# Kernel tuning notes

Hardware: AMD Instinct MI355X
Metric: run time of the kernel (lower is better)

The kernel has to match this reference:

```python
import jax, jax.numpy as jnp
import numpy as np

B, T, C = 8, 2048, 512

def setup_inputs() -> dict:
    key = jax.random.key(0)
    ks = jax.random.split(key, 16)
    def n(k, shape, s=0.02):
        return jax.random.normal(k, shape, dtype=jnp.float32) * s
    inp = {
        'x_l': jax.random.normal(ks[0], (B, T, C), jnp.float32),
        'x_r': jax.random.normal(ks[1], (B, T, C), jnp.float32),
    }
    i = 2
    for name in ['lp1', 'rp1', 'lp2', 'rp2']:
        inp[name + '_w1'] = n(ks[i], (C, C))       # pointwise conv1d weight (out,in)
        inp[name + '_b1'] = jnp.zeros((C,), jnp.float32)
        inp[name + '_w2'] = n(ks[i + 1], (C, 3))   # depthwise conv k=3 weight per channel
        inp[name + '_b2'] = jnp.zeros((C,), jnp.float32)
        i += 2
    inp['lp3_w'] = n(ks[i], (C, C)); inp['lp3_b'] = jnp.zeros((C,), jnp.float32)
    inp['rp3_w'] = n(ks[i + 1], (C, C)); inp['rp3_b'] = jnp.zeros((C,), jnp.float32)
    return inp

def _proj(x, w1, b1, w2, b2):
    # x: (B,T,C). Pointwise conv1d (1x1) then depthwise conv1d k=3, pad=1 over T.
    h = jnp.einsum('btc,dc->btd', x, w1) + b1
    hp = jnp.pad(h, ((0, 0), (1, 1), (0, 0)))
    # cross-correlation: tap 0 -> t-1, tap 1 -> t, tap 2 -> t+1 (matches torch Conv1d)
    return hp[:, :-2, :] * w2[:, 0] + hp[:, 1:-1, :] * w2[:, 1] + hp[:, 2:, :] * w2[:, 2] + b2

def reference(x_l, x_r,
              lp1_w1, lp1_b1, lp1_w2, lp1_b2,
              rp1_w1, rp1_b1, rp1_w2, rp1_b2,
              lp2_w1, lp2_b1, lp2_w2, lp2_b2,
              rp2_w1, rp2_b1, rp2_w2, rp2_b2,
              lp3_w, lp3_b, rp3_w, rp3_b):
    scale = C ** (-0.5)
    Q_l = _proj(x_l, lp1_w1, lp1_b1, lp1_w2, lp1_b2)  # (B,T,C)
    Q_r = _proj(x_r, rp1_w1, rp1_b1, rp1_w2, rp1_b2)  # (B,T,C)
    V_l = _proj(x_l, lp2_w1, lp2_b1, lp2_w2, lp2_b2)  # (B,T,C)
    V_r = _proj(x_r, rp2_w1, rp2_b1, rp2_w2, rp2_b2)  # (B,T,C)
    attn = jnp.einsum('btc,bsc->bts', Q_l, Q_r) * scale  # shared (B,T,T) scores
    # r->l: softmax over r-positions (last axis)
    F_r2l = jnp.einsum('bts,bsc->btc', jax.nn.softmax(attn, axis=-1), V_r)
    # l->r: softmax of attn^T over its last axis == softmax over axis 1 of attn
    F_l2r = jnp.einsum('bts,btc->bsc', jax.nn.softmax(attn, axis=1), V_l)
    out_l = x_l + jnp.einsum('btc,dc->btd', F_r2l, lp3_w) + lp3_b
    out_r = x_r + jnp.einsum('btc,dc->btd', F_l2r, rp3_w) + rp3_b
    return (out_l, out_r)
```

## Files before the change

kernel.cpp:

```cpp
#include <hip/hip_runtime.h>
#include <stdint.h>

#define Bb 8
#define Tt 2048
#define Cc 512

typedef __attribute__((ext_vector_type(8))) short short8;
typedef __attribute__((ext_vector_type(4))) short short4v;
typedef __attribute__((ext_vector_type(4))) float f32x4;

#define SZE ((size_t)Bb * Tt * Cc)

__device__ __forceinline__ float b2f(short s) {
  unsigned int x = ((unsigned int)(unsigned short)s) << 16;
  return __builtin_bit_cast(float, x);
}
__device__ __forceinline__ short f2b(float f) {
  unsigned int x = __builtin_bit_cast(unsigned int, f);
  x += 0x7fffu + ((x >> 16) & 1u);
  return (short)(x >> 16);
}

__device__ __forceinline__ void gload16(const void* g, void* l) {
  __builtin_amdgcn_global_load_lds(
      (const __attribute__((address_space(1))) void*)g,
      (__attribute__((address_space(3))) void*)l, 16, 0, 0);
}

template<int MODE>
__global__ __launch_bounds__(256, 2)
void gemm_bt(const void* __restrict__ Av, const void* __restrict__ Av2,
             const void* __restrict__ Bv, const void* __restrict__ Bv2,
             void* __restrict__ Cv, void* __restrict__ Cv2,
             const float* __restrict__ bias,
             const float* __restrict__ resid, const float* __restrict__ resid2,
             short* __restrict__ ET, float* __restrict__ sumR, float* __restrict__ sumC,
             int M, int N, int K,
             long long sA, long long sB, long long sC, float scale)
{
  __shared__ __align__(16) short ldsA[8 * 128 * 8];
  __shared__ __align__(16) short ldsB[8 * 128 * 8];
  const int tid  = threadIdx.x;
  const int lane = tid & 63;

  int bxi = blockIdx.x, byi = blockIdx.y, bzi = blockIdx.z;
  const int gx = gridDim.x, gy = gridDim.y;
  if ((gy & 7) == 0) {
    int l = bxi + gx * (byi + gy * bzi);
    const int xcd = l & 7;
    int loc = l >> 3;
    const int ych = gy >> 3;
    bxi = loc % gx;  loc /= gx;
    byi = xcd * ych + (loc % ych);
    bzi = loc / ych;
  }

  const int bm = byi * 128;
  const int bn = bxi * 128;
  int dir = 0, zz = bzi;
  if constexpr (MODE == 1 || MODE == 2) { dir = bzi >> 3; zz = bzi & 7; }
  const long long zoA = (long long)zz * sA;
  const long long zoB = (long long)zz * sB;
  const long long zoC = (long long)zz * sC;
  const void* Ause = Av;
  const void* Buse = Bv;
  void* Cuse = Cv;
  if constexpr (MODE == 0) {
    if (zz) Ause = Av2;
  }
  if constexpr (MODE == 1 || MODE == 2) {
    if (dir) { Ause = Av2; Buse = Bv2; Cuse = Cv2; }
  }

  const int wv = tid >> 6;
  const int wm = (wv >> 1) << 6;
  const int wn = (wv & 1) << 6;
  const int wvb = wv << 6;

  f32x4 zero4 = {0.f, 0.f, 0.f, 0.f};
  f32x4 acc[4][4];
#pragma unroll
  for (int i = 0; i < 4; ++i)
#pragma unroll
    for (int j = 0; j < 4; ++j)
      acc[i][j] = zero4;

  const int sm  = tid >> 3;
  const int skc = tid & 7;

  for (int k0 = 0; k0 < K; k0 += 64) {
    if constexpr (MODE == 0) {
#pragma unroll
      for (int r = 0; r < 4; ++r) {
        const int m = r * 32 + sm;
        const float* ap = (const float*)Ause + zoA + (size_t)(bm + m) * K + k0 + skc * 8;
        float4 f0 = *(const float4*)ap;
        float4 f1 = *(const float4*)(ap + 4);
        short8 av;
        av[0] = f2b(f0.x); av[1] = f2b(f0.y); av[2] = f2b(f0.z); av[3] = f2b(f0.w);
        av[4] = f2b(f1.x); av[5] = f2b(f1.y); av[6] = f2b(f1.z); av[7] = f2b(f1.w);
        *(short8*)&ldsA[((m << 3) + (skc ^ (m & 7))) << 3] = av;
      }
#pragma unroll
      for (int q = 0; q < 4; ++q) {
        const int d  = q * 256 + tid;
        const int mm = d >> 3;
        const int kc = (d & 7) ^ (mm & 7);
        gload16((const short*)Buse + zoB + (size_t)(bn + mm) * K + k0 + kc * 8,
                &ldsB[(size_t)(q * 256 + wvb) * 8]);
      }
    } else {
#pragma unroll
      for (int q = 0; q < 4; ++q) {
        const int d  = q * 256 + tid;
        const int mm = d >> 3;
        const int kc = (d & 7) ^ (mm & 7);
        const size_t ko = (size_t)k0 + kc * 8;
        gload16((const short*)Ause + zoA + (size_t)(bm + mm) * K + ko,
                &ldsA[(size_t)(q * 256 + wvb) * 8]);
        gload16((const short*)Buse + zoB + (size_t)(bn + mm) * K + ko,
                &ldsB[(size_t)(q * 256 + wvb) * 8]);
      }
    }
    __syncthreads();
#pragma unroll
    for (int kk = 0; kk < 2; ++kk) {
      const int kcr = (kk << 2) + (lane >> 4);
      short8 af[4], bfv[4];
#pragma unroll
      for (int i = 0; i < 4; ++i) {
        const int ma = wm + i * 16 + (lane & 15);
        const int nb = wn + i * 16 + (lane & 15);
        af[i]  = *(const short8*)&ldsA[((ma << 3) + (kcr ^ (ma & 7))) << 3];
        bfv[i] = *(const short8*)&ldsB[((nb << 3) + (kcr ^ (nb & 7))) << 3];
      }
#pragma unroll
      for (int i = 0; i < 4; ++i)
#pragma unroll
        for (int j = 0; j < 4; ++j)
          acc[i][j] = __builtin_amdgcn_mfma_f32_16x16x32_bf16(af[i], bfv[j], acc[i][j], 0, 0, 0);
    }
    __syncthreads();
  }

  if constexpr (MODE == 4) {
#pragma unroll
    for (int i = 0; i < 4; ++i)
#pragma unroll
      for (int j = 0; j < 4; ++j)
#pragma unroll
        for (int r = 0; r < 4; ++r)
          acc[i][j][r] = __expf(acc[i][j][r] * scale);

#pragma unroll
    for (int i = 0; i < 4; ++i) {
      const int row0 = bm + wm + i * 16 + ((lane >> 4) << 2);
#pragma unroll
      for (int j = 0; j < 4; ++j) {
        const int n = bn + wn + j * 16 + (lane & 15);
        short4v t;
#pragma unroll
        for (int r = 0; r < 4; ++r) t[r] = f2b(acc[i][j][r]);
#pragma unroll
        for (int r = 0; r < 4; ++r)
          ((short*)Cv)[zoC + (size_t)(row0 + r) * N + n] = t[r];
        *(short4v*)(ET + zoC + (size_t)n * M + row0) = t;
      }
    }
#pragma unroll
    for (int i = 0; i < 4; ++i) {
      const int row0 = bm + wm + i * 16 + ((lane >> 4) << 2);
#pragma unroll
      for (int r = 0; r < 4; ++r) {
        float p = acc[i][0][r] + acc[i][1][r] + acc[i][2][r] + acc[i][3][r];
#pragma unroll
        for (int o = 1; o < 16; o <<= 1) p += __shfl_xor(p, o, 64);
        if ((lane & 15) == 0)
          unsafeAtomicAdd(&sumR[(size_t)zz * M + row0 + r], p);
      }
    }
#pragma unroll
    for (int j = 0; j < 4; ++j) {
      const int n = bn + wn + j * 16 + (lane & 15);
      float q = 0.f;
#pragma unroll
      for (int i = 0; i < 4; ++i)
#pragma unroll
        for (int r = 0; r < 4; ++r) q += acc[i][j][r];
      q += __shfl_xor(q, 16, 64);
      q += __shfl_xor(q, 32, 64);
      if (lane < 16)
        unsafeAtomicAdd(&sumC[(size_t)zz * N + n], q);
    }
  } else if constexpr (MODE == 2) {
    const float* sums = dir ? sumC : sumR;
    const float* xr   = dir ? resid2 : resid;
#pragma unroll
    for (int i = 0; i < 4; ++i) {
      const int row0 = bm + wm + i * 16 + ((lane >> 4) << 2);
#pragma unroll
      for (int r = 0; r < 4; ++r) {
        const float iv = 1.0f / sums[(size_t)zz * M + row0 + r];
#pragma unroll
        for (int j = 0; j < 4; ++j) {
          const int n = bn + wn + j * 16 + (lane & 15);
          const size_t off = zoC + (size_t)(row0 + r) * N + n;
          ((float*)Cuse)[off] = acc[i][j][r] * iv + bias[dir * N + n] + xr[off];
        }
      }
    }
  } else {
#pragma unroll
    for (int i = 0; i < 4; ++i) {
      const int row0 = bm + wm + i * 16 + ((lane >> 4) << 2);
#pragma unroll
      for (int j = 0; j < 4; ++j) {
        const int n = bn + wn + j * 16 + (lane & 15);
        float badd = 0.f;
        if (MODE == 0) badd = bias[(size_t)zz * N + n];
#pragma unroll
        for (int r = 0; r < 4; ++r) {
          float val = acc[i][j][r];
          if (MODE == 0) val += badd;
          ((short*)Cuse)[zoC + (size_t)(row0 + r) * N + n] = f2b(val);
        }
      }
    }
  }
  (void)resid; (void)resid2; (void)ET; (void)sumR; (void)sumC;
  (void)bias; (void)scale; (void)Cuse; (void)M;
}

__global__ __launch_bounds__(256)
void pack_all(const float* __restrict__ lw1a, const float* __restrict__ lw1b,
              const float* __restrict__ rw1a, const float* __restrict__ rw1b,
              const float* __restrict__ w3lf, const float* __restrict__ w3rf,
              const float* __restrict__ lb1a, const float* __restrict__ lb1b,
              const float* __restrict__ rb1a, const float* __restrict__ rb1b,
              const float* __restrict__ b3l, const float* __restrict__ b3r,
              short* __restrict__ Wl, short* __restrict__ Wr,
              short* __restrict__ W3l, short* __restrict__ W3r,
              float* __restrict__ BL, float* __restrict__ BR,
              float* __restrict__ B3, float* __restrict__ SUM)
{
  const int i = blockIdx.x * 256 + threadIdx.x;
  if (i < 524288) {
    Wl[i] = f2b(i < 262144 ? lw1a[i] : lw1b[i - 262144]);
  } else if (i < 1048576) {
    const int j = i - 524288;
    Wr[j] = f2b(j < 262144 ? rw1a[j] : rw1b[j - 262144]);
  } else if (i < 1310720) {
    W3l[i - 1048576] = f2b(w3lf[i - 1048576]);
  } else if (i < 1572864) {
    W3r[i - 1310720] = f2b(w3rf[i - 1310720]);
  } else if (i < 1573888) {
    const int j = i - 1572864;
    BL[j] = j < 512 ? lb1a[j] : lb1b[j - 512];
  } else if (i < 1574912) {
    const int j = i - 1573888;
    BR[j] = j < 512 ? rb1a[j] : rb1b[j - 512];
  } else if (i < 1575936) {
    const int j = i - 1574912;
    B3[j] = j < 512 ? b3l[j] : b3r[j - 512];
  } else if (i < 1608704) {
    SUM[i - 1575936] = 0.f;
  }
}

__global__ __launch_bounds__(256)
void dw_kernel(const short* __restrict__ H, long long hStride,
               const float* __restrict__ w2a, const float* __restrict__ w2b,
               const float* __restrict__ w2c, const float* __restrict__ w2d,
               const float* __restrict__ b2a, const float* __restrict__ b2b,
               const float* __restrict__ b2c, const float* __restrict__ b2d,
               short* __restrict__ out)
{
  const int y = blockIdx.y;
  const short* Hd = H + (size_t)(y & 1) * hStride;
  const float* w2 = (y == 0) ? w2a : (y == 1) ? w2b : (y == 2) ? w2c : w2d;
  const float* b2 = (y == 0) ? b2a : (y == 1) ? b2b : (y == 2) ? b2c : b2d;
  const int colOff = (y & 2) ? 512 : 0;
  short* outd = out + (size_t)y * SZE;

  const int idx = blockIdx.x * 256 + threadIdx.x;
  const int c8 = idx & 63;
  const int bt = idx >> 6;
  const int t  = bt & (Tt - 1);
  const int c  = c8 << 3;
  const short* base = Hd + (size_t)bt * 1024 + colOff + c;
  short8 zv = {0, 0, 0, 0, 0, 0, 0, 0};
  short8 hm = zv, hp = zv;
  short8 h0 = *(const short8*)base;
  if (t > 0)      hm = *(const short8*)(base - 1024);
  if (t < Tt - 1) hp = *(const short8*)(base + 1024);
  short8 o;
#pragma unroll
  for (int j = 0; j < 8; ++j) {
    const int cj = c + j;
    float val = b2f(hm[j]) * w2[cj * 3 + 0]
              + b2f(h0[j]) * w2[cj * 3 + 1]
              + b2f(hp[j]) * w2[cj * 3 + 2]
              + b2[cj];
    o[j] = f2b(val);
  }
  *(short8*)(outd + (size_t)bt * Cc + c) = o;
}

extern "C" void kernel_launch(void* const* d_in, const int* in_sizes, int n_in,
                              void* d_out, int out_size, void* d_ws, size_t ws_size,
                              hipStream_t stream)
{
  const float* x_l    = (const float*)d_in[0];
  const float* x_r    = (const float*)d_in[1];
  const float* lp1_w1 = (const float*)d_in[2];
  const float* lp1_b1 = (const float*)d_in[3];
  const float* lp1_w2 = (const float*)d_in[4];
  const float* lp1_b2 = (const float*)d_in[5];
  const float* rp1_w1 = (const float*)d_in[6];
  const float* rp1_b1 = (const float*)d_in[7];
  const float* rp1_w2 = (const float*)d_in[8];
  const float* rp1_b2 = (const float*)d_in[9];
  const float* lp2_w1 = (const float*)d_in[10];
  const float* lp2_b1 = (const float*)d_in[11];
  const float* lp2_w2 = (const float*)d_in[12];
  const float* lp2_b2 = (const float*)d_in[13];
  const float* rp2_w1 = (const float*)d_in[14];
  const float* rp2_b1 = (const float*)d_in[15];
  const float* rp2_w2 = (const float*)d_in[16];
  const float* rp2_b2 = (const float*)d_in[17];
  const float* lp3_w  = (const float*)d_in[18];
  const float* lp3_b  = (const float*)d_in[19];
  const float* rp3_w  = (const float*)d_in[20];
  const float* rp3_b  = (const float*)d_in[21];

  short* ws = (short*)d_ws;
  const size_t SZ = SZE;
  short* Ql   = ws;
  short* Qr   = ws + SZ;
  short* Vl   = ws + 2 * SZ;
  short* Vr   = ws + 3 * SZ;
  short* E    = ws + 4 * SZ;
  short* ETb  = ws + 8 * SZ;
  short* H    = E;
  short* VWT0 = Ql;
  short* VWT1 = Qr;

  const size_t W_PAIR = 524288, W_SING = 262144;
  short* Wl  = ws + 12 * SZ;
  short* Wr  = Wl + W_PAIR;
  short* W3l = Wr + W_PAIR;
  short* W3r = W3l + W_SING;
  float* BL  = (float*)(W3r + W_SING);
  float* BR  = BL + 1024;
  float* B3  = BR + 1024;
  float* SUMR = B3 + 1024;
  float* SUMC = SUMR + 16384;

  const float scale = 0.04419417382415922f;
  const int MT = Bb * Tt;
  const long long sQ = (long long)Tt * Cc;
  const long long sS = (long long)Tt * Tt;

  dim3 blk(256);

  pack_all<<<6284, blk, 0, stream>>>(lp1_w1, lp2_w1, rp1_w1, rp2_w1, lp3_w, rp3_w,
                                     lp1_b1, lp2_b1, rp1_b1, rp2_b1, lp3_b, rp3_b,
                                     Wl, Wr, W3l, W3r, BL, BR, B3, SUMR);

  gemm_bt<0><<<dim3(8, 128, 2), blk, 0, stream>>>(
      x_l, x_r, Wl, nullptr, H, nullptr, BL, nullptr, nullptr,
      nullptr, nullptr, nullptr,
      MT, 1024, Cc, 0, (long long)W_PAIR, (long long)(2 * SZ), 1.f);
  dw_kernel<<<dim3(4096, 4), blk, 0, stream>>>(
      H, (long long)(2 * SZ),
      lp1_w2, rp1_w2, lp2_w2, rp2_w2,
      lp1_b2, rp1_b2, lp2_b2, rp2_b2, Ql);

  gemm_bt<4><<<dim3(Tt / 128, Tt / 128, Bb), blk, 0, stream>>>(
      Ql, nullptr, Qr, nullptr, E, nullptr, nullptr, nullptr, nullptr,
      ETb, SUMR, SUMC,
      Tt, Tt, Cc, sQ, sQ, sS, scale);

  gemm_bt<1><<<dim3(Tt / 128, 4, 2 * Bb), blk, 0, stream>>>(
      W3l, W3r, Vr, Vl, VWT0, VWT1, nullptr, nullptr, nullptr,
      nullptr, nullptr, nullptr,
      512, Tt, Cc, 0, sQ, (long long)(512 * Tt), 1.f);

  gemm_bt<2><<<dim3(Cc / 128, Tt / 128, 2 * Bb), blk, 0, stream>>>(
      E, ETb, VWT0, VWT1, d_out, (float*)d_out + SZ, B3, x_l, x_r,
      nullptr, SUMR, SUMC,
      Tt, Cc, Tt, sS, (long long)(512 * Tt), sQ, 1.f);

  (void)in_sizes; (void)n_in; (void)out_size; (void)ws_size;
}
```

Baseline: 428.5 us.

## Double-buffer LDS with async global-to-LDS prefetch in bf16 GEMM modes

For the non-fp32 GEMM modes, LDS becomes two buffers and the next-next K tile is prefetched with global_load_lds while MFMAs consume the current tile. Explicit vmcnt waits and raw s_barrier replace __syncthreads, which lets loads stay in flight across iterations. The aim is to hide global memory latency behind compute. In exchange it doubles LDS use to 64KB per block, which may limit the occupancy of 2 blocks per CU, and it depends on the vmcnt counting being exact.

```diff
diff --git a/kernel.cpp b/kernel.cpp
--- a/kernel.cpp
+++ b/kernel.cpp
@@ -38,8 +38,8 @@
              int M, int N, int K,
              long long sA, long long sB, long long sC, float scale)
 {
-  __shared__ __align__(16) short ldsA[8 * 128 * 8];
-  __shared__ __align__(16) short ldsB[8 * 128 * 8];
+  constexpr int NBUF = (MODE == 0) ? 1 : 2;
+  __shared__ __align__(16) short lds[NBUF][2][8192];
   const int tid  = threadIdx.x;
   const int lane = tid & 63;
 
@@ -88,8 +88,8 @@
   const int sm  = tid >> 3;
   const int skc = tid & 7;
 
-  for (int k0 = 0; k0 < K; k0 += 64) {
-    if constexpr (MODE == 0) {
+  if constexpr (MODE == 0) {
+    for (int k0 = 0; k0 < K; k0 += 64) {
 #pragma unroll
       for (int r = 0; r < 4; ++r) {
         const int m = r * 32 + sm;
@@ -99,7 +99,7 @@
         short8 av;
         av[0] = f2b(f0.x); av[1] = f2b(f0.y); av[2] = f2b(f0.z); av[3] = f2b(f0.w);
         av[4] = f2b(f1.x); av[5] = f2b(f1.y); av[6] = f2b(f1.z); av[7] = f2b(f1.w);
-        *(short8*)&ldsA[((m << 3) + (skc ^ (m & 7))) << 3] = av;
+        *(short8*)&lds[0][0][((m << 3) + (skc ^ (m & 7))) << 3] = av;
       }
 #pragma unroll
       for (int q = 0; q < 4; ++q) {
@@ -107,9 +107,30 @@
         const int mm = d >> 3;
         const int kc = (d & 7) ^ (mm & 7);
         gload16((const short*)Buse + zoB + (size_t)(bn + mm) * K + k0 + kc * 8,
-                &ldsB[(size_t)(q * 256 + wvb) * 8]);
-      }
-    } else {
+                &lds[0][1][(size_t)(q * 256 + wvb) * 8]);
+      }
+      __syncthreads();
+#pragma unroll
+      for (int kk = 0; kk < 2; ++kk) {
+        const int kcr = (kk << 2) + (lane >> 4);
+        short8 af[4], bfv[4];
+#pragma unroll
+        for (int i = 0; i < 4; ++i) {
+          const int ma = wm + i * 16 + (lane & 15);
+          const int nb = wn + i * 16 + (lane & 15);
+          af[i]  = *(const short8*)&lds[0][0][((ma << 3) + (kcr ^ (ma & 7))) << 3];
+          bfv[i] = *(const short8*)&lds[0][1][((nb << 3) + (kcr ^ (nb & 7))) << 3];
+        }
+#pragma unroll
+        for (int i = 0; i < 4; ++i)
+#pragma unroll
+          for (int j = 0; j < 4; ++j)
+            acc[i][j] = __builtin_amdgcn_mfma_f32_16x16x32_bf16(af[i], bfv[j], acc[i][j], 0, 0, 0);
+      }
+      __syncthreads();
+    }
+  } else {
+    auto stage = [&](int buf, int k0) {
 #pragma unroll
       for (int q = 0; q < 4; ++q) {
         const int d  = q * 256 + tid;
@@ -117,30 +138,43 @@
         const int kc = (d & 7) ^ (mm & 7);
         const size_t ko = (size_t)k0 + kc * 8;
         gload16((const short*)Ause + zoA + (size_t)(bm + mm) * K + ko,
-                &ldsA[(size_t)(q * 256 + wvb) * 8]);
+                &lds[buf][0][(size_t)(q * 256 + wvb) * 8]);
         gload16((const short*)Buse + zoB + (size_t)(bn + mm) * K + ko,
-                &ldsB[(size_t)(q * 256 + wvb) * 8]);
-      }
-    }
-    __syncthreads();
-#pragma unroll
-    for (int kk = 0; kk < 2; ++kk) {
-      const int kcr = (kk << 2) + (lane >> 4);
-      short8 af[4], bfv[4];
-#pragma unroll
-      for (int i = 0; i < 4; ++i) {
-        const int ma = wm + i * 16 + (lane & 15);
-        const int nb = wn + i * 16 + (lane & 15);
-        af[i]  = *(const short8*)&ldsA[((ma << 3) + (kcr ^ (ma & 7))) << 3];
-        bfv[i] = *(const short8*)&ldsB[((nb << 3) + (kcr ^ (nb & 7))) << 3];
-      }
-#pragma unroll
-      for (int i = 0; i < 4; ++i)
-#pragma unroll
-        for (int j = 0; j < 4; ++j)
-          acc[i][j] = __builtin_amdgcn_mfma_f32_16x16x32_bf16(af[i], bfv[j], acc[i][j], 0, 0, 0);
-    }
-    __syncthreads();
+                &lds[buf][1][(size_t)(q * 256 + wvb) * 8]);
+      }
+    };
+    const int nt = K >> 6;
+    stage(0, 0);
+    stage(1, 64);
+    int cur = 0;
+    for (int t = 0; t < nt; ++t) {
+      if (t < nt - 1) {
+        asm volatile("s_waitcnt vmcnt(8)" ::: "memory");
+      } else {
+        asm volatile("s_waitcnt vmcnt(0)" ::: "memory");
+      }
+      __builtin_amdgcn_s_barrier();
+#pragma unroll
+      for (int kk = 0; kk < 2; ++kk) {
+        const int kcr = (kk << 2) + (lane >> 4);
+        short8 af[4], bfv[4];
+#pragma unroll
+        for (int i = 0; i < 4; ++i) {
+          const int ma = wm + i * 16 + (lane & 15);
+          const int nb = wn + i * 16 + (lane & 15);
+          af[i]  = *(const short8*)&lds[cur][0][((ma << 3) + (kcr ^ (ma & 7))) << 3];
+          bfv[i] = *(const short8*)&lds[cur][1][((nb << 3) + (kcr ^ (nb & 7))) << 3];
+        }
+#pragma unroll
+        for (int i = 0; i < 4; ++i)
+#pragma unroll
+          for (int j = 0; j < 4; ++j)
+            acc[i][j] = __builtin_amdgcn_mfma_f32_16x16x32_bf16(af[i], bfv[j], acc[i][j], 0, 0, 0);
+      }
+      __builtin_amdgcn_s_barrier();
+      if (t + 2 < nt) stage(cur, (t + 2) << 6);
+      cur ^= 1;
+    }
   }
 
   if constexpr (MODE == 4) {
```

New measurement: 432.1 us. No clear change (+0.8%).
